# Kernel tuning notes

Measured on AMD Instinct MI355X. Metric: run time of the kernel, lower is better.

The kernel has to match this reference:

```python
import jax, jax.numpy as jnp
import numpy as np

B, T, HID = 2, 1024, 4096
H, D_NOPE, D_ROPE, D_V = 32, 128, 64, 128
D_QK = D_NOPE + D_ROPE  # 192
Q_RANK, KV_RANK = 1536, 512
THETA, EPS = 10000.0, 1e-6
SCALE = D_QK ** -0.5
NEG = -1e30


def rms_norm(x, w):
    return x * jax.lax.rsqrt(jnp.mean(x * x, axis=-1, keepdims=True) + EPS) * w


def apply_rope(x, positions):
    # x: [B, T, h, d] (d even), positions: [B, T]
    d = x.shape[-1]
    inv_freq = 1.0 / (THETA ** (jnp.arange(0, d, 2, dtype=jnp.float32) / d))
    ang = positions.astype(jnp.float32)[:, :, None, None] * inv_freq  # [B,T,1,d/2]
    cos, sin = jnp.cos(ang), jnp.sin(ang)
    x1, x2 = jnp.split(x, 2, axis=-1)
    return jnp.concatenate([x1 * cos - x2 * sin, x1 * sin + x2 * cos], axis=-1)


def setup_inputs() -> dict:
    key = jax.random.key(0)
    ks = jax.random.split(key, 8)
    def lin(k, fan_in, fan_out):
        return (jax.random.normal(k, (fan_in, fan_out), jnp.float32)
                / np.float32(np.sqrt(fan_in)))
    return {
        "x": jax.random.normal(ks[0], (B, T, HID), jnp.float32),
        "wq_a": lin(ks[1], HID, Q_RANK),
        "q_norm_w": jnp.ones((Q_RANK,), jnp.float32),
        "wq_b": lin(ks[2], Q_RANK, H * D_QK),
        "wkv_a": lin(ks[3], HID, KV_RANK + D_ROPE),
        "kv_norm_w": jnp.ones((KV_RANK,), jnp.float32),
        "wkv_b": lin(ks[4], KV_RANK, H * (D_NOPE + D_V)),
        "wo": lin(ks[5], H * D_V, HID),
        "attention_mask": jnp.ones((B, T), jnp.int32),
        "positions": jnp.broadcast_to(jnp.arange(T, dtype=jnp.int32), (B, T)),
    }


def reference(x, wq_a, q_norm_w, wq_b, wkv_a, kv_norm_w, wkv_b, wo,
              attention_mask, positions):
    # ---- query path: low-rank down-proj, RMSNorm, up-proj ----
    q = rms_norm(x @ wq_a, q_norm_w) @ wq_b           # [B,T,H*D_QK]
    q = q.reshape(B, T, H, D_QK)
    q_nope, q_pe = jnp.split(q, [D_NOPE], axis=-1)
    q_pe = apply_rope(q_pe, positions)                # [B,T,H,D_ROPE]

    # ---- kv path: compressed latent + shared rope key ----
    kv_out = x @ wkv_a                                # [B,T,KV_RANK+D_ROPE]
    kv, k_pe = jnp.split(kv_out, [KV_RANK], axis=-1)
    k_pe = apply_rope(k_pe[:, :, None, :], positions) # [B,T,1,D_ROPE]
    kv_exp = rms_norm(kv, kv_norm_w) @ wkv_b          # [B,T,H*(D_NOPE+D_V)]
    kv_exp = kv_exp.reshape(B, T, H, D_NOPE + D_V)
    k_nope, v = jnp.split(kv_exp, [D_NOPE], axis=-1)

    q = jnp.concatenate([q_nope, q_pe], axis=-1)      # [B,T,H,D_QK]
    k = jnp.concatenate(
        [k_nope, jnp.broadcast_to(k_pe, (B, T, H, D_ROPE))], axis=-1)

    # ---- attention (causal + padding mask) ----
    scores = jnp.einsum('bthd,bshd->bhts', q, k) * SCALE     # [B,H,T,T]
    causal = jnp.tril(jnp.ones((T, T), dtype=bool))
    mask = causal[None, None] & (attention_mask[:, None, None, :] != 0)
    scores = jnp.where(mask, scores, NEG)
    attn = jax.nn.softmax(scores, axis=-1)
    out = jnp.einsum('bhts,bshd->bthd', attn, v)              # [B,T,H,D_V]
    return out.reshape(B, T, H * D_V) @ wo                    # [B,T,HID]
```

## Files before the change

### kernel.cpp

```cpp
#include <hip/hip_runtime.h>
#include <hip/hip_bf16.h>

#define BB 2
#define TT 1024
#define HIDD 4096
#define NH 32
#define DN 128
#define DR 64
#define DVV 128
#define DQK 192
#define QR 1536
#define KVR 512
#define MTOK (BB*TT)
#define EPSF 1e-6f
#define SCALEF 0.07216878364870322f

typedef unsigned short u16;
using bfrag = __attribute__((ext_vector_type(8))) short;
using f4 = __attribute__((ext_vector_type(4))) float;

__device__ __forceinline__ float bf2f(u16 u){
    union { unsigned int i; float f; } v; v.i = ((unsigned int)u) << 16; return v.f;
}
__device__ __forceinline__ u16 f2bf(float f){
    union { float f; unsigned int i; } v; v.f = f;
    unsigned int r = v.i + 0x7fffu + ((v.i >> 16) & 1u);
    return (u16)(r >> 16);
}
__device__ __forceinline__ void async16(const void* g, void* l){
    __builtin_amdgcn_global_load_lds((const __attribute__((address_space(1))) void*)g,
                                     (__attribute__((address_space(3))) void*)l, 16, 0, 0);
}

__global__ __launch_bounds__(256) void cvt_k(const float* __restrict__ in,
                                             u16* __restrict__ out, int n)
{
    int i = (blockIdx.x * 256 + threadIdx.x) * 4;
    if (i >= n) return;
    float4 v = *(const float4*)(in + i);
    ushort4 o = make_ushort4(f2bf(v.x), f2bf(v.y), f2bf(v.z), f2bf(v.w));
    *(ushort4*)(out + i) = o;
}

__global__ __launch_bounds__(256) void transpose_cvt(
    const float* __restrict__ W, u16* __restrict__ Wt, int Kd, int Nd)
{
    __shared__ u16 S[32][33];
    const int n0 = blockIdx.x * 32, k0 = blockIdx.y * 32;
    const int tx = threadIdx.x & 31, ty = threadIdx.x >> 5;
    #pragma unroll
    for (int i = 0; i < 4; ++i)
        S[ty + 8 * i][tx] = f2bf(W[(size_t)(k0 + ty + 8 * i) * Nd + n0 + tx]);
    __syncthreads();
    #pragma unroll
    for (int i = 0; i < 4; ++i)
        Wt[(size_t)(n0 + ty + 8 * i) * Kd + k0 + tx] = S[tx][ty + 8 * i];
}

template<int BN, int CMODE>
__global__ __launch_bounds__(256) void gemm_bt(
    const u16* __restrict__ A, const u16* __restrict__ Bt, void* __restrict__ C,
    u16* __restrict__ C2, int M, int N, int K, int lda)
{
    constexpr int BM = 128, BK = 64;
    constexpr int WAVES_N = (BN == 128) ? 2 : 1;
    constexpr int WAVES_M = 4 / WAVES_N;
    constexpr int WM = BM / WAVES_M, WN = BN / WAVES_N;
    constexpr int FM = WM / 16, FN = WN / 16;
    constexpr int AISS = (BM * BK / 8) / 256;
    constexpr int BISS = (BN * BK / 8) / 256;
    __shared__ alignas(16) u16 As[2][BM * BK];
    __shared__ alignas(16) u16 Bs[2][BN * BK];
    const int tid = threadIdx.x, w = tid >> 6, ln = tid & 63;
    const int row0 = blockIdx.y * BM, col0 = blockIdx.x * BN;
    const int wm = w / WAVES_N, wn = w % WAVES_N;
    const int lr = ln & 15, lq = ln >> 4;
    const int sw = lr & 7;

    f4 acc[FM][FN];
    #pragma unroll
    for (int i = 0; i < FM; ++i)
        #pragma unroll
        for (int j = 0; j < FN; ++j)
            acc[i][j] = (f4){0.f, 0.f, 0.f, 0.f};

    const int srow = ln >> 3;
    const int scol = ((ln & 7) ^ srow) * 8;
    const u16* pA = A + (size_t)(row0 + w * (AISS * 8) + srow) * lda + scol;
    const u16* pB = Bt + (size_t)(col0 + w * (BISS * 8) + srow) * K + scol;

    auto stageA = [&](int buf, int k0) {
        #pragma unroll
        for (int i = 0; i < AISS; ++i)
            async16(pA + (size_t)i * 8 * lda + k0, &As[buf][(w * AISS + i) * 512]);
    };
    auto stageB = [&](int buf, int k0) {
        #pragma unroll
        for (int i = 0; i < BISS; ++i)
            async16(pB + (size_t)i * 8 * K + k0, &Bs[buf][(w * BISS + i) * 512]);
    };

    stageA(0, 0); stageB(0, 0);
    __syncthreads();

    const int nkt = K / BK;
    int cur = 0;
    for (int kt = 0; kt < nkt; ++kt) {
        if (kt + 1 < nkt) { stageA(cur ^ 1, (kt + 1) * BK); stageB(cur ^ 1, (kt + 1) * BK); }
        #pragma unroll
        for (int ks = 0; ks < 2; ++ks) {
            const int sl = ((ks * 4 + lq) ^ sw) * 8;
            bfrag af[FM], bfr[FN];
            #pragma unroll
            for (int fm = 0; fm < FM; ++fm)
                af[fm] = *(const bfrag*)&As[cur][(wm * WM + fm * 16 + lr) * BK + sl];
            #pragma unroll
            for (int fn = 0; fn < FN; ++fn)
                bfr[fn] = *(const bfrag*)&Bs[cur][(wn * WN + fn * 16 + lr) * BK + sl];
            #pragma unroll
            for (int fm = 0; fm < FM; ++fm)
                #pragma unroll
                for (int fn = 0; fn < FN; ++fn)
                    acc[fm][fn] = __builtin_amdgcn_mfma_f32_16x16x32_bf16(
                        af[fm], bfr[fn], acc[fm][fn], 0, 0, 0);
        }
        __syncthreads();
        cur ^= 1;
    }
    #pragma unroll
    for (int fm = 0; fm < FM; ++fm)
        #pragma unroll
        for (int fn = 0; fn < FN; ++fn) {
            const int col = col0 + wn * WN + fn * 16 + lr;
            const int rowb = row0 + wm * WM + fm * 16 + lq * 4;
            if (CMODE == 2) {
                const int head = col >> 8, within = col & 255;
                if (within < DN) {
                    #pragma unroll
                    for (int r = 0; r < 4; ++r)
                        ((u16*)C)[(size_t)(rowb + r) * (NH * DN) + head * DN + within]
                            = f2bf(acc[fm][fn][r]);
                } else {
                    ushort4 pk = make_ushort4(f2bf(acc[fm][fn][0]), f2bf(acc[fm][fn][1]),
                                              f2bf(acc[fm][fn][2]), f2bf(acc[fm][fn][3]));
                    size_t off = ((size_t)((rowb >> 10) * NH + head) * DVV + (within - DN)) * TT
                                 + (rowb & (TT - 1));
                    *(ushort4*)(C2 + off) = pk;
                }
            } else {
                #pragma unroll
                for (int r = 0; r < 4; ++r) {
                    size_t off = (size_t)(rowb + r) * N + col;
                    if (CMODE == 1) ((float*)C)[off] = acc[fm][fn][r];
                    else            ((u16*)C)[off] = f2bf(acc[fm][fn][r]);
                }
            }
        }
}

__global__ __launch_bounds__(256) void rmsnorm_bf(
    u16* __restrict__ p, const float* __restrict__ w, int W, int stride)
{
    u16* x = p + (size_t)blockIdx.x * stride;
    __shared__ float red[256];
    float s = 0.f;
    for (int c = threadIdx.x; c < W; c += 256) { float v = bf2f(x[c]); s += v * v; }
    red[threadIdx.x] = s;
    __syncthreads();
    for (int off = 128; off > 0; off >>= 1) {
        if (threadIdx.x < off) red[threadIdx.x] += red[threadIdx.x + off];
        __syncthreads();
    }
    float scale = rsqrtf(red[0] / (float)W + EPSF);
    for (int c = threadIdx.x; c < W; c += 256)
        x[c] = f2bf(bf2f(x[c]) * scale * w[c]);
}

__global__ void rope_q_k(u16* __restrict__ q, const int* __restrict__ pos)
{
    int idx = blockIdx.x * 256 + threadIdx.x;
    if (idx >= MTOK * NH * 32) return;
    int j = idx & 31, h = (idx >> 5) & 31, tok = idx >> 10;
    u16* p = q + (size_t)tok * (NH * DQK) + h * DQK + DN;
    float x1 = bf2f(p[j]), x2 = bf2f(p[j + 32]);
    float inv = __expf((float)j * -0.28782313662425572f);
    float ang = (float)pos[tok] * inv;
    float sn, cs; sincosf(ang, &sn, &cs);
    p[j] = f2bf(x1 * cs - x2 * sn);
    p[j + 32] = f2bf(x1 * sn + x2 * cs);
}

__global__ void rope_k_k(const u16* __restrict__ kvd, u16* __restrict__ kpe,
                         const int* __restrict__ pos)
{
    int idx = blockIdx.x * 256 + threadIdx.x;
    if (idx >= MTOK * 32) return;
    int j = idx & 31, tok = idx >> 5;
    const u16* p = kvd + (size_t)tok * 576 + KVR;
    float x1 = bf2f(p[j]), x2 = bf2f(p[j + 32]);
    float inv = __expf((float)j * -0.28782313662425572f);
    float ang = (float)pos[tok] * inv;
    float sn, cs; sincosf(ang, &sn, &cs);
    kpe[(size_t)tok * 64 + j] = f2bf(x1 * cs - x2 * sn);
    kpe[(size_t)tok * 64 + j + 32] = f2bf(x1 * sn + x2 * cs);
}

struct SMa {
    alignas(16) u16 Ks[2][64 * 192];
    alignas(16) u16 Ps[4][16 * 72];
};
struct SMb { alignas(16) u16 Ot[64 * 136]; };
union SMu { SMa a; SMb o; };

__global__ __launch_bounds__(256, 2) void attn_mfma(
    const u16* __restrict__ q, const u16* __restrict__ KN,
    const u16* __restrict__ kpe, const u16* __restrict__ VT,
    const int* __restrict__ amask, u16* __restrict__ O)
{
    __shared__ SMu sm;
    const int tid = threadIdx.x, w = tid >> 6, ln = tid & 63;
    const int lr = ln & 15, lq = ln >> 4;
    const int h = blockIdx.x, b = blockIdx.z;
    const u16* vtb = VT + (size_t)(b * NH + h) * DVV * TT;

    auto stage = [&](u16* dst, int k0) {
        #pragma unroll
        for (int i = 0; i < 6; ++i) {
            const int p = (w * 6 + i) * 64 + ln;
            const int row = p / 24;
            const int c = (p - row * 24) ^ (row & 7);
            const int col = c << 3;
            const u16* src = (col < DN)
                ? KN + (size_t)(b * TT + k0 + row) * (NH * DN) + h * DN + col
                : kpe + (size_t)(b * TT + k0 + row) * 64 + (col - DN);
            async16(src, dst + (w * 6 + i) * 512);
        }
    };

    #pragma unroll
    for (int pass = 0; pass < 2; ++pass) {
        const int t = pass ? (15 - blockIdx.y) : blockIdx.y;
        const int q0 = t * 64;
        const int qg0 = q0 + w * 16 + lq * 4;

        bfrag qf[6];
        const u16* qbase = q + (size_t)(b * TT + q0 + w * 16 + lr) * (NH * DQK) + h * DQK + lq * 8;
        #pragma unroll
        for (int ks = 0; ks < 6; ++ks) qf[ks] = *(const bfrag*)(qbase + ks * 32);

        f4 acc[8];
        #pragma unroll
        for (int i = 0; i < 8; ++i) acc[i] = (f4){0.f, 0.f, 0.f, 0.f};
        float m_i[4], l_i[4];
        #pragma unroll
        for (int r = 0; r < 4; ++r) { m_i[r] = -1e30f; l_i[r] = 0.f; }

        __syncthreads();
        stage(sm.a.Ks[0], 0);
        __syncthreads();

        u16* cur = sm.a.Ks[0];
        u16* nxt = sm.a.Ks[1];
        const int nkt = t + 1;
        for (int kt = 0; kt < nkt; ++kt) {
            const int k0 = kt * 64;

            float mb[4];
            #pragma unroll
            for (int nt = 0; nt < 4; ++nt)
                mb[nt] = amask[b * TT + k0 + nt * 16 + lr] ? 0.f : -1e30f;
            bfrag vf0[8], vf1[8];
            #pragma unroll
            for (int d = 0; d < 8; ++d) {
                const u16* vrow = vtb + (size_t)(d * 16 + lr) * TT + k0 + lq * 8;
                vf0[d] = *(const bfrag*)vrow;
                vf1[d] = *(const bfrag*)(vrow + 32);
            }
            if (kt + 1 < nkt) stage(nxt, k0 + 64);

            f4 sacc[4];
            #pragma unroll
            for (int nt = 0; nt < 4; ++nt) {
                sacc[nt] = (f4){0.f, 0.f, 0.f, 0.f};
                const int r_ = nt * 16 + lr;
                const u16* kr = cur + r_ * 192;
                const int sw = r_ & 7;
                #pragma unroll
                for (int ks = 0; ks < 6; ++ks) {
                    bfrag kf = *(const bfrag*)(kr + (((ks * 4 + lq) ^ sw) << 3));
                    sacc[nt] = __builtin_amdgcn_mfma_f32_16x16x32_bf16(qf[ks], kf, sacc[nt], 0, 0, 0);
                }
            }

            float s[4][4];
            #pragma unroll
            for (int nt = 0; nt < 4; ++nt) {
                const int keyg = k0 + nt * 16 + lr;
                #pragma unroll
                for (int r = 0; r < 4; ++r) {
                    float v = sacc[nt][r] * SCALEF + mb[nt];
                    s[nt][r] = (keyg <= qg0 + r) ? v : -1e30f;
                }
            }
            #pragma unroll
            for (int r = 0; r < 4; ++r) {
                float tm = fmaxf(fmaxf(s[0][r], s[1][r]), fmaxf(s[2][r], s[3][r]));
                tm = fmaxf(tm, __shfl_xor(tm, 1));
                tm = fmaxf(tm, __shfl_xor(tm, 2));
                tm = fmaxf(tm, __shfl_xor(tm, 4));
                tm = fmaxf(tm, __shfl_xor(tm, 8));
                float m_new = fmaxf(m_i[r], tm);
                float alpha = __expf(m_i[r] - m_new);
                float p0 = __expf(s[0][r] - m_new);
                float p1 = __expf(s[1][r] - m_new);
                float p2 = __expf(s[2][r] - m_new);
                float p3 = __expf(s[3][r] - m_new);
                float rs = (p0 + p1) + (p2 + p3);
                rs += __shfl_xor(rs, 1);
                rs += __shfl_xor(rs, 2);
                rs += __shfl_xor(rs, 4);
                rs += __shfl_xor(rs, 8);
                l_i[r] = l_i[r] * alpha + rs;
                m_i[r] = m_new;
                #pragma unroll
                for (int d = 0; d < 8; ++d) acc[d][r] *= alpha;
                sm.a.Ps[w][(lq * 4 + r) * 72 + lr] = f2bf(p0);
                sm.a.Ps[w][(lq * 4 + r) * 72 + 16 + lr] = f2bf(p1);
                sm.a.Ps[w][(lq * 4 + r) * 72 + 32 + lr] = f2bf(p2);
                sm.a.Ps[w][(lq * 4 + r) * 72 + 48 + lr] = f2bf(p3);
            }
            bfrag pf0 = *(const bfrag*)&sm.a.Ps[w][lr * 72 + lq * 8];
            bfrag pf1 = *(const bfrag*)&sm.a.Ps[w][lr * 72 + 32 + lq * 8];
            #pragma unroll
            for (int d = 0; d < 8; ++d) {
                acc[d] = __builtin_amdgcn_mfma_f32_16x16x32_bf16(pf0, vf0[d], acc[d], 0, 0, 0);
                acc[d] = __builtin_amdgcn_mfma_f32_16x16x32_bf16(pf1, vf1[d], acc[d], 0, 0, 0);
            }
            __syncthreads();
            u16* tmp = cur; cur = nxt; nxt = tmp;
        }
        float inv_l[4];
        #pragma unroll
        for (int r = 0; r < 4; ++r) inv_l[r] = 1.0f / l_i[r];
        #pragma unroll
        for (int d = 0; d < 8; ++d)
            #pragma unroll
            for (int r = 0; r < 4; ++r)
                sm.o.Ot[(w * 16 + lq * 4 + r) * 136 + d * 16 + lr] = f2bf(acc[d][r] * inv_l[r]);
        __syncthreads();
        #pragma unroll
        for (int it = 0; it < 8; ++it) {
            int u = it * 256 + tid;
            int orow = u >> 5, ocol = (u & 31) * 4;
            ushort4 o4 = *(const ushort4*)&sm.o.Ot[orow * 136 + ocol];
            *(ushort4*)&O[(size_t)(b * TT + q0 + orow) * (NH * DVV) + h * DVV + ocol] = o4;
        }
    }
}

extern "C" void kernel_launch(void* const* d_in, const int* in_sizes, int n_in,
                              void* d_out, int out_size, void* d_ws, size_t ws_size,
                              hipStream_t stream)
{
    const float* x      = (const float*)d_in[0];
    const float* wq_a   = (const float*)d_in[1];
    const float* q_nw   = (const float*)d_in[2];
    const float* wq_b   = (const float*)d_in[3];
    const float* wkv_a  = (const float*)d_in[4];
    const float* kv_nw  = (const float*)d_in[5];
    const float* wkv_b  = (const float*)d_in[6];
    const float* wo     = (const float*)d_in[7];
    const int* amask    = (const int*)d_in[8];
    const int* pos      = (const int*)d_in[9];

    u16* ws = (u16*)d_ws;
    u16* wqa_t  = ws;
    u16* wqb_t  = wqa_t  + (size_t)QR * HIDD;
    u16* wkva_t = wqb_t  + (size_t)NH * DQK * QR;
    u16* wkvb_t = wkva_t + (size_t)576 * HIDD;
    u16* wo_t   = wkvb_t + (size_t)NH * 256 * KVR;
    u16* xb     = wo_t   + (size_t)HIDD * HIDD;
    u16* q_down = xb     + (size_t)MTOK * HIDD;
    u16* qbuf   = q_down + (size_t)MTOK * QR;
    u16* kvd    = qbuf   + (size_t)MTOK * NH * DQK;
    u16* kpe    = kvd    + (size_t)MTOK * 576;
    u16* KN     = kpe    + (size_t)MTOK * 64;
    u16* VT     = KN     + (size_t)MTOK * NH * DN;
    u16* Obuf   = wqa_t;

    cvt_k<<<(MTOK*HIDD/4 + 255)/256, 256, 0, stream>>>(x, xb, MTOK*HIDD);
    transpose_cvt<<<dim3(QR/32, HIDD/32), 256, 0, stream>>>(wq_a, wqa_t, HIDD, QR);
    transpose_cvt<<<dim3(NH*DQK/32, QR/32), 256, 0, stream>>>(wq_b, wqb_t, QR, NH*DQK);
    transpose_cvt<<<dim3(576/32, HIDD/32), 256, 0, stream>>>(wkv_a, wkva_t, HIDD, 576);
    transpose_cvt<<<dim3(NH*256/32, KVR/32), 256, 0, stream>>>(wkv_b, wkvb_t, KVR, NH*256);
    transpose_cvt<<<dim3(HIDD/32, HIDD/32), 256, 0, stream>>>(wo, wo_t, HIDD, HIDD);

    gemm_bt<128, 0><<<dim3(QR/128, MTOK/128), 256, 0, stream>>>(
        xb, wqa_t, q_down, nullptr, MTOK, QR, HIDD, HIDD);
    gemm_bt<64, 0><<<dim3(576/64, MTOK/128), 256, 0, stream>>>(
        xb, wkva_t, kvd, nullptr, MTOK, 576, HIDD, HIDD);
    rmsnorm_bf<<<MTOK, 256, 0, stream>>>(q_down, q_nw, QR, QR);
    rmsnorm_bf<<<MTOK, 256, 0, stream>>>(kvd, kv_nw, KVR, 576);
    rope_k_k<<<(MTOK*32 + 255)/256, 256, 0, stream>>>(kvd, kpe, pos);
    gemm_bt<128, 0><<<dim3(NH*DQK/128, MTOK/128), 256, 0, stream>>>(
        q_down, wqb_t, qbuf, nullptr, MTOK, NH*DQK, QR, QR);
    gemm_bt<128, 2><<<dim3(NH*256/128, MTOK/128), 256, 0, stream>>>(
        kvd, wkvb_t, KN, VT, MTOK, NH*256, KVR, 576);
    rope_q_k<<<(MTOK*NH*32 + 255)/256, 256, 0, stream>>>(qbuf, pos);
    attn_mfma<<<dim3(NH, 8, BB), 256, 0, stream>>>(qbuf, KN, kpe, VT, amask, Obuf);
    gemm_bt<128, 1><<<dim3(HIDD/128, MTOK/128), 256, 0, stream>>>(
        Obuf, wo_t, (float*)d_out, nullptr, MTOK, HIDD, NH*DVV, NH*DVV);
}
```

Before: 586.2 us.

## Split attention KV loop across two blocks and merge partials with combine kernel

The attention kernel now splits each query tile's key tiles between two blocks by interleaving kt parity. Each block writes a partial normalized output plus its row max and sum, and a new combine kernel merges them with softmax rescaling. This doubles the grid and, with a single K buffer, lets launch bounds rise to 4 blocks per SM to raise occupancy. In exchange the K staging is no longer double-buffered and sits behind syncs every tile, and the change adds extra partial-output traffic and a kernel launch.

```diff
diff --git a/kernel.cpp b/kernel.cpp
--- a/kernel.cpp
+++ b/kernel.cpp
@@ -206,24 +206,27 @@
 }
 
 struct SMa {
-    alignas(16) u16 Ks[2][64 * 192];
+    alignas(16) u16 Ks[64 * 192];
     alignas(16) u16 Ps[4][16 * 72];
 };
 struct SMb { alignas(16) u16 Ot[64 * 136]; };
 union SMu { SMa a; SMb o; };
 
-__global__ __launch_bounds__(256, 2) void attn_mfma(
+__global__ __launch_bounds__(256, 4) void attn_mfma(
     const u16* __restrict__ q, const u16* __restrict__ KN,
     const u16* __restrict__ kpe, const u16* __restrict__ VT,
-    const int* __restrict__ amask, u16* __restrict__ O)
+    const int* __restrict__ amask, u16* __restrict__ Opart, float* __restrict__ ml)
 {
     __shared__ SMu sm;
     const int tid = threadIdx.x, w = tid >> 6, ln = tid & 63;
     const int lr = ln & 15, lq = ln >> 4;
-    const int h = blockIdx.x, b = blockIdx.z;
+    const int h = blockIdx.x;
+    const int b = blockIdx.z & 1, sp = blockIdx.z >> 1;
     const u16* vtb = VT + (size_t)(b * NH + h) * DVV * TT;
-
-    auto stage = [&](u16* dst, int k0) {
+    u16* opb = Opart + (size_t)sp * MTOK * NH * DVV;
+    float* mlb = ml + (size_t)sp * MTOK * NH * 2;
+
+    auto stage = [&](int k0) {
         #pragma unroll
         for (int i = 0; i < 6; ++i) {
             const int p = (w * 6 + i) * 64 + ln;
@@ -233,7 +236,7 @@
             const u16* src = (col < DN)
                 ? KN + (size_t)(b * TT + k0 + row) * (NH * DN) + h * DN + col
                 : kpe + (size_t)(b * TT + k0 + row) * 64 + (col - DN);
-            async16(src, dst + (w * 6 + i) * 512);
+            async16(src, sm.a.Ks + (w * 6 + i) * 512);
         }
     };
 
@@ -255,16 +258,10 @@
         #pragma unroll
         for (int r = 0; r < 4; ++r) { m_i[r] = -1e30f; l_i[r] = 0.f; }
 
-        __syncthreads();
-        stage(sm.a.Ks[0], 0);
-        __syncthreads();
-
-        u16* cur = sm.a.Ks[0];
-        u16* nxt = sm.a.Ks[1];
-        const int nkt = t + 1;
-        for (int kt = 0; kt < nkt; ++kt) {
+        for (int kt = sp; kt <= t; kt += 2) {
             const int k0 = kt * 64;
-
+            __syncthreads();
+            stage(k0);
             float mb[4];
             #pragma unroll
             for (int nt = 0; nt < 4; ++nt)
@@ -276,14 +273,14 @@
                 vf0[d] = *(const bfrag*)vrow;
                 vf1[d] = *(const bfrag*)(vrow + 32);
             }
-            if (kt + 1 < nkt) stage(nxt, k0 + 64);
+            __syncthreads();
 
             f4 sacc[4];
             #pragma unroll
             for (int nt = 0; nt < 4; ++nt) {
                 sacc[nt] = (f4){0.f, 0.f, 0.f, 0.f};
                 const int r_ = nt * 16 + lr;
-                const u16* kr = cur + r_ * 192;
+                const u16* kr = sm.a.Ks + r_ * 192;
                 const int sw = r_ & 7;
                 #pragma unroll
                 for (int ks = 0; ks < 6; ++ks) {
@@ -336,12 +333,19 @@
                 acc[d] = __builtin_amdgcn_mfma_f32_16x16x32_bf16(pf0, vf0[d], acc[d], 0, 0, 0);
                 acc[d] = __builtin_amdgcn_mfma_f32_16x16x32_bf16(pf1, vf1[d], acc[d], 0, 0, 0);
             }
-            __syncthreads();
-            u16* tmp = cur; cur = nxt; nxt = tmp;
         }
         float inv_l[4];
         #pragma unroll
-        for (int r = 0; r < 4; ++r) inv_l[r] = 1.0f / l_i[r];
+        for (int r = 0; r < 4; ++r) inv_l[r] = (l_i[r] > 0.f) ? 1.0f / l_i[r] : 0.f;
+        if (lr == 0) {
+            #pragma unroll
+            for (int r = 0; r < 4; ++r) {
+                size_t mi = ((size_t)(b * TT + qg0 + r) * NH + h) * 2;
+                mlb[mi] = m_i[r];
+                mlb[mi + 1] = l_i[r];
+            }
+        }
+        __syncthreads();
         #pragma unroll
         for (int d = 0; d < 8; ++d)
             #pragma unroll
@@ -353,9 +357,32 @@
             int u = it * 256 + tid;
             int orow = u >> 5, ocol = (u & 31) * 4;
             ushort4 o4 = *(const ushort4*)&sm.o.Ot[orow * 136 + ocol];
-            *(ushort4*)&O[(size_t)(b * TT + q0 + orow) * (NH * DVV) + h * DVV + ocol] = o4;
+            *(ushort4*)&opb[(size_t)(b * TT + q0 + orow) * (NH * DVV) + h * DVV + ocol] = o4;
         }
     }
+}
+
+__global__ __launch_bounds__(256) void attn_combine(
+    const u16* __restrict__ Opart, const float* __restrict__ ml, u16* __restrict__ O)
+{
+    const size_t NPART = (size_t)MTOK * NH * DVV;
+    size_t e = ((size_t)blockIdx.x * 256 + threadIdx.x) * 8;
+    const int tok = (int)(e >> 12);
+    const int h = ((int)(e >> 7)) & 31;
+    const float* p0 = ml + ((size_t)tok * NH + h) * 2;
+    const float* p1 = ml + (((size_t)MTOK + tok) * NH + h) * 2;
+    float m0 = p0[0], l0 = p0[1], m1 = p1[0], l1 = p1[1];
+    float M = fmaxf(m0, m1);
+    float w0 = l0 * __expf(m0 - M), w1 = l1 * __expf(m1 - M);
+    float inv = 1.0f / (w0 + w1);
+    w0 *= inv; w1 *= inv;
+    bfrag a = *(const bfrag*)(Opart + e);
+    bfrag c = *(const bfrag*)(Opart + NPART + e);
+    bfrag r;
+    #pragma unroll
+    for (int i = 0; i < 8; ++i)
+        r[i] = (short)f2bf(w0 * bf2f((u16)a[i]) + w1 * bf2f((u16)c[i]));
+    *(bfrag*)(O + e) = r;
 }
 
 extern "C" void kernel_launch(void* const* d_in, const int* in_sizes, int n_in,
@@ -386,7 +413,9 @@
     u16* kpe    = kvd    + (size_t)MTOK * 576;
     u16* KN     = kpe    + (size_t)MTOK * 64;
     u16* VT     = KN     + (size_t)MTOK * NH * DN;
-    u16* Obuf   = wqa_t;
+    u16* Opart  = wqa_t;
+    float* mlbuf = (float*)kvd;
+    u16* Obuf   = xb;
 
     cvt_k<<<(MTOK*HIDD/4 + 255)/256, 256, 0, stream>>>(x, xb, MTOK*HIDD);
     transpose_cvt<<<dim3(QR/32, HIDD/32), 256, 0, stream>>>(wq_a, wqa_t, HIDD, QR);
@@ -407,7 +436,8 @@
     gemm_bt<128, 2><<<dim3(NH*256/128, MTOK/128), 256, 0, stream>>>(
         kvd, wkvb_t, KN, VT, MTOK, NH*256, KVR, 576);
     rope_q_k<<<(MTOK*NH*32 + 255)/256, 256, 0, stream>>>(qbuf, pos);
-    attn_mfma<<<dim3(NH, 8, BB), 256, 0, stream>>>(qbuf, KN, kpe, VT, amask, Obuf);
+    attn_mfma<<<dim3(NH, 8, BB*2), 256, 0, stream>>>(qbuf, KN, kpe, VT, amask, Opart, mlbuf);
+    attn_combine<<<(MTOK*NH*DVV/8)/256, 256, 0, stream>>>(Opart, mlbuf, Obuf);
     gemm_bt<128, 1><<<dim3(HIDD/128, MTOK/128), 256, 0, stream>>>(
         Obuf, wo_t, (float*)d_out, nullptr, MTOK, HIDD, NH*DVV, NH*DVV);
 }
```

New measurement: 800.6 us. +36.6%, slower.
